# Kernel optimization log

Hardware: AMD Instinct MI355X
Metric: run time of the kernel (lower is better)

Reference implementation:

```python
import math
import jax, jax.numpy as jnp
import numpy as np

D_MODEL = 1024
H_HEADS = 16
D_K = D_MODEL // H_HEADS


def setup_inputs() -> dict:
    key = jax.random.key(0)
    ks = jax.random.split(key, 7)
    B, L = 4, 2048
    q = jax.random.normal(ks[0], (B, L, D_MODEL), dtype=jnp.float32)
    k = jax.random.normal(ks[1], (B, L, D_MODEL), dtype=jnp.float32)
    v = jax.random.normal(ks[2], (B, L, D_MODEL), dtype=jnp.float32)
    mask = jnp.ones((1, L, L), dtype=jnp.int32)
    # nn.Linear(d_model, d_model, bias=False) weights, shape (out, in)
    s = 1.0 / math.sqrt(D_MODEL)
    W_q = jax.random.uniform(ks[3], (D_MODEL, D_MODEL), jnp.float32, -s, s)
    W_k = jax.random.uniform(ks[4], (D_MODEL, D_MODEL), jnp.float32, -s, s)
    W_v = jax.random.uniform(ks[5], (D_MODEL, D_MODEL), jnp.float32, -s, s)
    W_o = jax.random.uniform(ks[6], (D_MODEL, D_MODEL), jnp.float32, -s, s)
    return {"q": q, "k": k, "v": v, "mask": mask,
            "W_q": W_q, "W_k": W_k, "W_v": W_v, "W_o": W_o}


def reference(q, k, v, mask, W_q, W_k, W_v, W_o):
    B, Lq, _ = q.shape
    # projections (Linear: x @ W.T) then split heads -> (B, H, L, d_k)
    def split_heads(x):
        return x.reshape(B, -1, H_HEADS, D_K).transpose(0, 2, 1, 3)
    Q = split_heads(jnp.einsum('bsd,ed->bse', q, W_q))
    K = split_heads(jnp.einsum('bsd,ed->bse', k, W_k))
    V = split_heads(jnp.einsum('bsd,ed->bse', v, W_v))
    # scores: (B, H, Lq, Lk)
    scores = jnp.einsum('bhqd,bhkd->bhqk', Q, K) / math.sqrt(D_K)
    m = mask[:, None, :, :]  # (1, 1, Lq, Lk) broadcast
    scores = jnp.where(m == 0, -jnp.inf, scores)
    weights = jax.nn.softmax(scores, axis=-1)
    attn = jnp.einsum('bhqk,bhkd->bhqd', weights, V)  # (B, H, Lq, d_v)
    attn = attn.transpose(0, 2, 1, 3).reshape(B, Lq, D_MODEL)
    return jnp.einsum('bse,de->bsd', attn, W_o)
```

## Files before the change

### kernel.cpp

```cpp
#include <hip/hip_runtime.h>
#include <hip/hip_bf16.h>


typedef unsigned short u16;
typedef float f32x4  __attribute__((ext_vector_type(4)));
typedef float f32x16 __attribute__((ext_vector_type(16)));
typedef short s16x8  __attribute__((ext_vector_type(8)));
typedef unsigned u32x4 __attribute__((ext_vector_type(4)));
typedef __bf16 bf16x8 __attribute__((ext_vector_type(8)));

#define QSCL 0.18033688011112042f

__device__ __forceinline__ u16 f2b(float f) {
    union { float f; unsigned u; } x; x.f = f;
    unsigned r = x.u + 0x7fffu + ((x.u >> 16) & 1u);
    return (u16)(r >> 16);
}

__device__ __forceinline__ f32x4 MF(s16x8 a, s16x8 b, f32x4 c) {
    return __builtin_amdgcn_mfma_f32_16x16x32_bf16(
        __builtin_bit_cast(bf16x8, a), __builtin_bit_cast(bf16x8, b), c, 0, 0, 0);
}
__device__ __forceinline__ f32x16 MF32(s16x8 a, s16x8 b, f32x16 c) {
    return __builtin_amdgcn_mfma_f32_32x32x16_bf16(
        __builtin_bit_cast(bf16x8, a), __builtin_bit_cast(bf16x8, b), c, 0, 0, 0);
}
__device__ __forceinline__ unsigned cvtpk(float lo, float hi) {
    unsigned r;
    asm("v_cvt_pk_bf16_f32 %0, %1, %2" : "=v"(r) : "v"(lo), "v"(hi));
    return r;
}
__device__ __forceinline__ void swap32(unsigned &a, unsigned &b) {
    asm volatile("v_permlane32_swap_b32 %0, %1" : "+v"(a), "+v"(b));
}
__device__ __forceinline__ float expa(float x) {
    float r;
    asm("v_exp_f32 %0, %1" : "=v"(r) : "v"(x));
    return r;
}
__device__ __forceinline__ void g2l16(const u16* g, u16* lbase) {
    __builtin_amdgcn_global_load_lds((const __attribute__((address_space(1))) void*)g,
                                     (__attribute__((address_space(3))) void*)lbase, 16, 0, 0);
}

__global__ __launch_bounds__(256)
void mask_flags(const int* __restrict__ mask, int* __restrict__ mflag) {
    __shared__ int anyz;
    if (threadIdx.x == 0) anyz = 0;
    __syncthreads();
    const int qt = blockIdx.x >> 4, kt = blockIdx.x & 15;
    int local = 0;
#pragma unroll
    for (int q = 0; q < 16; ++q) {
        int e4 = q * 256 + threadIdx.x;
        int r = e4 >> 5, cc = (e4 & 31) * 4;
        int4 mv = *(const int4*)(mask + (size_t)(qt * 128 + r) * 2048 + kt * 128 + cc);
        local |= (mv.x == 0) | (mv.y == 0) | (mv.z == 0) | (mv.w == 0);
    }
    if (local) atomicOr(&anyz, 1);
    __syncthreads();
    if (threadIdx.x == 0) mflag[blockIdx.x] = anyz;
}

__global__ __launch_bounds__(256)
void convert_all(const float* __restrict__ q, const float* __restrict__ k,
                 const float* __restrict__ v, const float* __restrict__ Wq,
                 const float* __restrict__ Wk, const float* __restrict__ Wv,
                 const float* __restrict__ Wo, u16* __restrict__ Abf,
                 u16* __restrict__ Wbf) {
    const size_t NQKV = 25165824;
    const size_t NCH  = 3670016;
    for (size_t cidx = (size_t)blockIdx.x * 256 + threadIdx.x; cidx < NCH;
         cidx += (size_t)gridDim.x * 256) {
        size_t e = cidx * 8;
        const float* src; u16* dst; float scl = 1.f;
        if (e < NQKV) {
            src = (e < 8388608) ? q + e
                : (e < 16777216) ? k + (e - 8388608) : v + (e - 16777216);
            dst = Abf + e;
        } else {
            size_t o = e - NQKV;
            if (o < 1048576)      { src = Wq + o; scl = QSCL; }
            else if (o < 2097152) { src = Wk + (o - 1048576); }
            else if (o < 3145728) { src = Wv + (o - 2097152); }
            else                  { src = Wo + (o - 3145728); }
            dst = Wbf + o;
        }
        float4 a = *(const float4*)(src);
        float4 b = *(const float4*)(src + 4);
        ushort4 p0, p1;
        p0.x = f2b(a.x * scl); p0.y = f2b(a.y * scl);
        p0.z = f2b(a.z * scl); p0.w = f2b(a.w * scl);
        p1.x = f2b(b.x * scl); p1.y = f2b(b.y * scl);
        p1.z = f2b(b.z * scl); p1.w = f2b(b.w * scl);
        *(ushort4*)dst = p0; *(ushort4*)(dst + 4) = p1;
    }
}

__global__ __launch_bounds__(256)
void gemm_qkv_fast(const u16* __restrict__ Abf, const u16* __restrict__ Wbf,
                   u16* __restrict__ Qh, u16* __restrict__ Kf, u16* __restrict__ Vf) {
    __shared__ __align__(16) u16 As[128 * 32];
    __shared__ __align__(16) u16 Bs[128 * 32];
    const int z = blockIdx.z;
    const u16* A = Abf + (size_t)z * (8192 * 1024);
    const u16* W = Wbf + (size_t)z * (1024 * 1024);
    const int tid = threadIdx.x, l = tid & 63, w = tid >> 6;
    const int g = l >> 4, c = l & 15;
    const int m0 = blockIdx.y * 128, n0 = blockIdx.x * 128;
    const int wr = (w >> 1) * 64, wc = (w & 1) * 64;

    f32x4 acc[4][4];
#pragma unroll
    for (int i = 0; i < 4; ++i)
#pragma unroll
        for (int j = 0; j < 4; ++j)
#pragma unroll
            for (int e = 0; e < 4; ++e) acc[i][j][e] = 0.f;

    const u16* Ag = A + (size_t)(m0 + w * 32 + (l >> 2)) * 1024 + (l & 3) * 8;
    const u16* Wg = W + (size_t)(n0 + w * 32 + (l >> 2)) * 1024 + (l & 3) * 8;
    u16* Al = As + w * 1024;
    u16* Bl = Bs + w * 1024;

    for (int kt = 0; kt < 32; ++kt) {
        __syncthreads();
        g2l16(Ag + kt * 32,         Al);
        g2l16(Ag + kt * 32 + 16384, Al + 512);
        g2l16(Wg + kt * 32,         Bl);
        g2l16(Wg + kt * 32 + 16384, Bl + 512);
        __syncthreads();
        s16x8 af[4], bf[4];
#pragma unroll
        for (int i = 0; i < 4; ++i) {
            af[i] = *(const s16x8*)(As + (wr + i * 16 + c) * 32 + g * 8);
            bf[i] = *(const s16x8*)(Bs + (wc + i * 16 + c) * 32 + g * 8);
        }
#pragma unroll
        for (int mi = 0; mi < 4; ++mi)
#pragma unroll
            for (int ni = 0; ni < 4; ++ni)
                acc[mi][ni] = MF(af[mi], bf[ni], acc[mi][ni]);
    }

    if (z == 0) {
#pragma unroll
        for (int mi = 0; mi < 4; ++mi)
#pragma unroll
            for (int ni = 0; ni < 4; ++ni)
#pragma unroll
                for (int j = 0; j < 4; ++j) {
                    int row = m0 + wr + mi * 16 + g * 4 + j;
                    int col = n0 + wc + ni * 16 + c;
                    int b = row >> 11, sl = row & 2047;
                    int h = col >> 6, d = col & 63;
                    Qh[(((size_t)(b * 16 + h)) * 2048 + sl) * 64 + d] = f2b(acc[mi][ni][j]);
                }
    } else if (z == 1) {
#pragma unroll
        for (int mi = 0; mi < 4; ++mi)
#pragma unroll
            for (int ni = 0; ni < 4; ++ni)
#pragma unroll
                for (int j = 0; j < 4; ++j) {
                    int row = m0 + wr + mi * 16 + g * 4 + j;
                    int col = n0 + wc + ni * 16 + c;
                    int b = row >> 11, kk = row & 2047;
                    int h = col >> 6, d = col & 63;
                    size_t off = (size_t)(b * 16 + h) * 131072
                               + (size_t)(((kk >> 5) * 4 + (d >> 4))) * 512
                               + ((kk & 31) + 32 * ((d >> 3) & 1)) * 8 + (d & 7);
                    Kf[off] = f2b(acc[mi][ni][j]);
                }
    } else {
#pragma unroll
        for (int mi = 0; mi < 4; ++mi)
#pragma unroll
            for (int ni = 0; ni < 4; ++ni) {
                int key0 = m0 + wr + mi * 16 + g * 4;
                int col  = n0 + wc + ni * 16 + c;
                int b = key0 >> 11, kk0 = key0 & 2047;
                int h = col >> 6, d = col & 63;
                size_t off = (size_t)(b * 16 + h) * 131072
                           + (size_t)((kk0 >> 6) * 8 + (d >> 5) * 4 + ((kk0 >> 4) & 3)) * 512
                           + (((kk0 >> 3) & 1) * 32 + (d & 31)) * 8 + (kk0 & 7);
                ushort4 pk;
                pk.x = f2b(acc[mi][ni][0]); pk.y = f2b(acc[mi][ni][1]);
                pk.z = f2b(acc[mi][ni][2]); pk.w = f2b(acc[mi][ni][3]);
                *(ushort4*)(Vf + off) = pk;
            }
    }
}

__global__ __launch_bounds__(256)
void gemm_out_fast(const u16* __restrict__ Ab, const u16* __restrict__ W,
                   float* __restrict__ Cout) {
    __shared__ __align__(16) u16 As[128 * 32];
    __shared__ __align__(16) u16 Bs[128 * 32];
    const int tid = threadIdx.x, l = tid & 63, w = tid >> 6;
    const int g = l >> 4, c = l & 15;
    const int m0 = blockIdx.y * 128, n0 = blockIdx.x * 128;
    const int wr = (w >> 1) * 64, wc = (w & 1) * 64;

    f32x4 acc[4][4];
#pragma unroll
    for (int i = 0; i < 4; ++i)
#pragma unroll
        for (int j = 0; j < 4; ++j)
#pragma unroll
            for (int e = 0; e < 4; ++e) acc[i][j][e] = 0.f;

    const u16* Ag = Ab + (size_t)(m0 + w * 32 + (l >> 2)) * 1024 + (l & 3) * 8;
    const u16* Wg = W  + (size_t)(n0 + w * 32 + (l >> 2)) * 1024 + (l & 3) * 8;
    u16* Al = As + w * 1024;
    u16* Bl = Bs + w * 1024;

    for (int kt = 0; kt < 32; ++kt) {
        __syncthreads();
        g2l16(Ag + kt * 32,         Al);
        g2l16(Ag + kt * 32 + 16384, Al + 512);
        g2l16(Wg + kt * 32,         Bl);
        g2l16(Wg + kt * 32 + 16384, Bl + 512);
        __syncthreads();
        s16x8 af[4], bf[4];
#pragma unroll
        for (int i = 0; i < 4; ++i) {
            af[i] = *(const s16x8*)(As + (wr + i * 16 + c) * 32 + g * 8);
            bf[i] = *(const s16x8*)(Bs + (wc + i * 16 + c) * 32 + g * 8);
        }
#pragma unroll
        for (int mi = 0; mi < 4; ++mi)
#pragma unroll
            for (int ni = 0; ni < 4; ++ni)
                acc[mi][ni] = MF(af[mi], bf[ni], acc[mi][ni]);
    }

#pragma unroll
    for (int mi = 0; mi < 4; ++mi)
#pragma unroll
        for (int ni = 0; ni < 4; ++ni)
#pragma unroll
            for (int j = 0; j < 4; ++j) {
                int row = m0 + wr + mi * 16 + g * 4 + j;
                int col = n0 + wc + ni * 16 + c;
                Cout[(size_t)row * 1024 + col] = acc[mi][ni][j];
            }
}

__global__ __launch_bounds__(256)
void flash_attn(const u16* __restrict__ Qh, const u16* __restrict__ Kf,
                const u16* __restrict__ Vf, const int* __restrict__ mask,
                const int* __restrict__ mflag, u16* __restrict__ attnB) {
    __shared__ __align__(16) u16 KV[2][2][8][512];

    const int tid = threadIdx.x, w = tid >> 6, l = tid & 63;
    const int hi = l >> 5, q32 = l & 31;
    const int bh = blockIdx.x, qt = blockIdx.y;
    const size_t base = (size_t)bh * (2048 * 64);
    const u16* Qp = Qh + base;
    const u16* Kp = Kf + base;
    const u16* Vp = Vf + base;
    const int qrow_w = qt * 128 + w * 32;

    s16x8 Qf[4];
#pragma unroll
    for (int s = 0; s < 4; ++s)
        Qf[s] = *(const s16x8*)(Qp + (size_t)(qrow_w + q32) * 64 + s * 16 + hi * 8);

    f32x16 z16;
#pragma unroll
    for (int r = 0; r < 16; ++r) z16[r] = 0.f;
    f32x16 oA = z16, oB = z16;
    float la[4] = {0.f, 0.f, 0.f, 0.f};

    auto stage = [&](int buf, int kt) {
        const u16* ks = Kp + (size_t)(kt * 8 + w * 2) * 512 + l * 8;
        const u16* vs = Vp + (size_t)(kt * 8 + w * 2) * 512 + l * 8;
        g2l16(ks,       &KV[buf][0][w * 2][0]);
        g2l16(ks + 512, &KV[buf][0][w * 2 + 1][0]);
        g2l16(vs,       &KV[buf][1][w * 2][0]);
        g2l16(vs + 512, &KV[buf][1][w * 2 + 1][0]);
    };
    stage(0, 0);

    for (int kt = 0; kt < 32; ++kt) {
        const int cur = kt & 1;
        __syncthreads();
        if (kt < 31) stage(cur ^ 1, kt + 1);

        __builtin_amdgcn_s_setprio(1);
        f32x16 sA, sB;
        {
            s16x8 ka = *(const s16x8*)&KV[cur][0][0][l * 8];
            s16x8 kb = *(const s16x8*)&KV[cur][0][4][l * 8];
            sA = MF32(ka, Qf[0], z16);
            sB = MF32(kb, Qf[0], z16);
        }
#pragma unroll
        for (int s = 1; s < 4; ++s) {
            s16x8 ka = *(const s16x8*)&KV[cur][0][s][l * 8];
            s16x8 kb = *(const s16x8*)&KV[cur][0][4 + s][l * 8];
            sA = MF32(ka, Qf[s], sA);
            sB = MF32(kb, Qf[s], sB);
        }
        __builtin_amdgcn_s_setprio(0);

        if (mflag[qt * 16 + (kt >> 1)] != 0) {
            const int qr = qrow_w + q32, kr0 = kt * 64;
#pragma unroll
            for (int r = 0; r < 16; ++r) {
                int key = (r & 3) + 8 * (r >> 2) + 4 * hi;
                if (mask[(size_t)qr * 2048 + kr0 + key] == 0)      sA[r] = -1e30f;
                if (mask[(size_t)qr * 2048 + kr0 + 32 + key] == 0) sB[r] = -1e30f;
            }
        }

#pragma unroll
        for (int r = 0; r < 16; ++r) { sA[r] = expa(sA[r]); la[r & 3] += sA[r]; }
#pragma unroll
        for (int r = 0; r < 16; ++r) { sB[r] = expa(sB[r]); la[r & 3] += sB[r]; }

        s16x8 Xp[4];
        {
            u32x4 t;
            unsigned a0 = cvtpk(sA[0], sA[1]),   a1 = cvtpk(sA[2], sA[3]);
            unsigned b0 = cvtpk(sA[4], sA[5]),   b1 = cvtpk(sA[6], sA[7]);
            swap32(a0, b0); swap32(a1, b1);
            t.x = a0; t.y = a1; t.z = b0; t.w = b1; Xp[0] = __builtin_bit_cast(s16x8, t);
            unsigned c0 = cvtpk(sA[8], sA[9]),   c1 = cvtpk(sA[10], sA[11]);
            unsigned d0 = cvtpk(sA[12], sA[13]), d1 = cvtpk(sA[14], sA[15]);
            swap32(c0, d0); swap32(c1, d1);
            t.x = c0; t.y = c1; t.z = d0; t.w = d1; Xp[1] = __builtin_bit_cast(s16x8, t);
            unsigned e0 = cvtpk(sB[0], sB[1]),   e1 = cvtpk(sB[2], sB[3]);
            unsigned f0 = cvtpk(sB[4], sB[5]),   f1 = cvtpk(sB[6], sB[7]);
            swap32(e0, f0); swap32(e1, f1);
            t.x = e0; t.y = e1; t.z = f0; t.w = f1; Xp[2] = __builtin_bit_cast(s16x8, t);
            unsigned g0 = cvtpk(sB[8], sB[9]),   g1 = cvtpk(sB[10], sB[11]);
            unsigned h0 = cvtpk(sB[12], sB[13]), h1 = cvtpk(sB[14], sB[15]);
            swap32(g0, h0); swap32(g1, h1);
            t.x = g0; t.y = g1; t.z = h0; t.w = h1; Xp[3] = __builtin_bit_cast(s16x8, t);
        }

        __builtin_amdgcn_s_setprio(1);
#pragma unroll
        for (int ks = 0; ks < 4; ++ks) {
            s16x8 v0 = *(const s16x8*)&KV[cur][1][ks][l * 8];
            s16x8 v1 = *(const s16x8*)&KV[cur][1][4 + ks][l * 8];
            oA = MF32(Xp[ks], v0, oA);
            oB = MF32(Xp[ks], v1, oB);
        }
        __builtin_amdgcn_s_setprio(0);
    }

    float ls = (la[0] + la[1]) + (la[2] + la[3]);
    ls += __shfl_xor(ls, 32);

    const int b = bh >> 4, h = bh & 15;
#pragma unroll
    for (int r = 0; r < 16; ++r) {
        int qloc = (r & 3) + 8 * (r >> 2) + 4 * hi;
        float lr = __shfl(ls, qloc);
        float inv = __builtin_amdgcn_rcpf(lr);
        int row = qt * 128 + w * 32 + qloc;
        u16* dst = attnB + ((size_t)b * 2048 + row) * 1024 + h * 64 + q32;
        dst[0]  = f2b(oA[r] * inv);
        dst[32] = f2b(oB[r] * inv);
    }
}

extern "C" void kernel_launch(void* const* d_in, const int* in_sizes, int n_in,
                              void* d_out, int out_size, void* d_ws, size_t ws_size,
                              hipStream_t stream) {
    const float* q    = (const float*)d_in[0];
    const float* k    = (const float*)d_in[1];
    const float* v    = (const float*)d_in[2];
    const int*   mask = (const int*)d_in[3];
    const float* Wq   = (const float*)d_in[4];
    const float* Wk   = (const float*)d_in[5];
    const float* Wv   = (const float*)d_in[6];
    const float* Wo   = (const float*)d_in[7];

    char* ws = (char*)d_ws;
    u16* Abf   = (u16*)(ws);
    u16* Wbf   = (u16*)(ws + (48u << 20));
    u16* Qh    = (u16*)(ws + (56u << 20));
    u16* Kf    = (u16*)(ws + (72u << 20));
    u16* Vf    = (u16*)(ws + (88u << 20));
    u16* attnB = (u16*)(ws);
    int* mflag = (int*)(ws + (104u << 20));

    mask_flags<<<dim3(256), dim3(256), 0, stream>>>(mask, mflag);
    convert_all<<<dim3(2048), dim3(256), 0, stream>>>(q, k, v, Wq, Wk, Wv, Wo, Abf, Wbf);
    gemm_qkv_fast<<<dim3(8, 64, 3), dim3(256), 0, stream>>>(Abf, Wbf, Qh, Kf, Vf);
    flash_attn<<<dim3(64, 16), dim3(256), 0, stream>>>(Qh, Kf, Vf, mask, mflag, attnB);
    gemm_out_fast<<<dim3(8, 64), dim3(256), 0, stream>>>(attnB, Wbf + 3145728, (float*)d_out);
}
```

Baseline: 235.4 us.

## Give each attention wave two query sub-tiles and swap GEMM grid axes

The flash attention kernel now runs 128 threads with each wave owning 64 query rows (two 32-row sub-tiles). Each K/V fragment read from shared memory is therefore reused for twice as many MFMAs, and each wave stages four K/V slabs instead of two. It also hoists a per-block any-mask check out of the loop. The two projection GEMMs swap their grid x/y mapping so that consecutive blocks walk along M rather than N, which changes L2 reuse of the weight tiles. The trade-off is higher register pressure and fewer waves per block in attention.

```diff
diff --git a/kernel.cpp b/kernel.cpp
--- a/kernel.cpp
+++ b/kernel.cpp
@@ -107,7 +107,7 @@
     const u16* W = Wbf + (size_t)z * (1024 * 1024);
     const int tid = threadIdx.x, l = tid & 63, w = tid >> 6;
     const int g = l >> 4, c = l & 15;
-    const int m0 = blockIdx.y * 128, n0 = blockIdx.x * 128;
+    const int m0 = blockIdx.x * 128, n0 = blockIdx.y * 128;
     const int wr = (w >> 1) * 64, wc = (w & 1) * 64;
 
     f32x4 acc[4][4];
@@ -199,7 +199,7 @@
     __shared__ __align__(16) u16 Bs[128 * 32];
     const int tid = threadIdx.x, l = tid & 63, w = tid >> 6;
     const int g = l >> 4, c = l & 15;
-    const int m0 = blockIdx.y * 128, n0 = blockIdx.x * 128;
+    const int m0 = blockIdx.x * 128, n0 = blockIdx.y * 128;
     const int wr = (w >> 1) * 64, wc = (w & 1) * 64;
 
     f32x4 acc[4][4];
@@ -247,7 +247,7 @@
             }
 }
 
-__global__ __launch_bounds__(256)
+__global__ __launch_bounds__(128)
 void flash_attn(const u16* __restrict__ Qh, const u16* __restrict__ Kf,
                 const u16* __restrict__ Vf, const int* __restrict__ mask,
                 const int* __restrict__ mflag, u16* __restrict__ attnB) {
@@ -260,26 +260,33 @@
     const u16* Qp = Qh + base;
     const u16* Kp = Kf + base;
     const u16* Vp = Vf + base;
-    const int qrow_w = qt * 128 + w * 32;
-
-    s16x8 Qf[4];
-#pragma unroll
-    for (int s = 0; s < 4; ++s)
-        Qf[s] = *(const s16x8*)(Qp + (size_t)(qrow_w + q32) * 64 + s * 16 + hi * 8);
+    const int qrow_w = qt * 128 + w * 64;
+
+    int anyflag = 0;
+#pragma unroll
+    for (int i = 0; i < 16; ++i) anyflag |= mflag[qt * 16 + i];
+
+    s16x8 Qf0[4], Qf1[4];
+#pragma unroll
+    for (int s = 0; s < 4; ++s) {
+        Qf0[s] = *(const s16x8*)(Qp + (size_t)(qrow_w + q32) * 64 + s * 16 + hi * 8);
+        Qf1[s] = *(const s16x8*)(Qp + (size_t)(qrow_w + 32 + q32) * 64 + s * 16 + hi * 8);
+    }
 
     f32x16 z16;
 #pragma unroll
     for (int r = 0; r < 16; ++r) z16[r] = 0.f;
-    f32x16 oA = z16, oB = z16;
-    float la[4] = {0.f, 0.f, 0.f, 0.f};
+    f32x16 oA0 = z16, oB0 = z16, oA1 = z16, oB1 = z16;
+    float la0[4] = {0.f, 0.f, 0.f, 0.f}, la1[4] = {0.f, 0.f, 0.f, 0.f};
 
     auto stage = [&](int buf, int kt) {
-        const u16* ks = Kp + (size_t)(kt * 8 + w * 2) * 512 + l * 8;
-        const u16* vs = Vp + (size_t)(kt * 8 + w * 2) * 512 + l * 8;
-        g2l16(ks,       &KV[buf][0][w * 2][0]);
-        g2l16(ks + 512, &KV[buf][0][w * 2 + 1][0]);
-        g2l16(vs,       &KV[buf][1][w * 2][0]);
-        g2l16(vs + 512, &KV[buf][1][w * 2 + 1][0]);
+        const u16* ks = Kp + (size_t)(kt * 8 + w * 4) * 512 + l * 8;
+        const u16* vs = Vp + (size_t)(kt * 8 + w * 4) * 512 + l * 8;
+#pragma unroll
+        for (int i = 0; i < 4; ++i) {
+            g2l16(ks + i * 512, &KV[buf][0][w * 4 + i][0]);
+            g2l16(vs + i * 512, &KV[buf][1][w * 4 + i][0]);
+        }
     };
     stage(0, 0);
 
@@ -289,56 +296,81 @@
         if (kt < 31) stage(cur ^ 1, kt + 1);
 
         __builtin_amdgcn_s_setprio(1);
-        f32x16 sA, sB;
+        f32x16 sA0, sB0, sA1, sB1;
         {
             s16x8 ka = *(const s16x8*)&KV[cur][0][0][l * 8];
             s16x8 kb = *(const s16x8*)&KV[cur][0][4][l * 8];
-            sA = MF32(ka, Qf[0], z16);
-            sB = MF32(kb, Qf[0], z16);
+            sA0 = MF32(ka, Qf0[0], z16); sA1 = MF32(ka, Qf1[0], z16);
+            sB0 = MF32(kb, Qf0[0], z16); sB1 = MF32(kb, Qf1[0], z16);
         }
 #pragma unroll
         for (int s = 1; s < 4; ++s) {
             s16x8 ka = *(const s16x8*)&KV[cur][0][s][l * 8];
             s16x8 kb = *(const s16x8*)&KV[cur][0][4 + s][l * 8];
-            sA = MF32(ka, Qf[s], sA);
-            sB = MF32(kb, Qf[s], sB);
+            sA0 = MF32(ka, Qf0[s], sA0); sA1 = MF32(ka, Qf1[s], sA1);
+            sB0 = MF32(kb, Qf0[s], sB0); sB1 = MF32(kb, Qf1[s], sB1);
         }
         __builtin_amdgcn_s_setprio(0);
 
-        if (mflag[qt * 16 + (kt >> 1)] != 0) {
-            const int qr = qrow_w + q32, kr0 = kt * 64;
+        if (anyflag && mflag[qt * 16 + (kt >> 1)] != 0) {
+            const int kr0 = kt * 64;
+            const int qr0 = qrow_w + q32, qr1 = qrow_w + 32 + q32;
 #pragma unroll
             for (int r = 0; r < 16; ++r) {
                 int key = (r & 3) + 8 * (r >> 2) + 4 * hi;
-                if (mask[(size_t)qr * 2048 + kr0 + key] == 0)      sA[r] = -1e30f;
-                if (mask[(size_t)qr * 2048 + kr0 + 32 + key] == 0) sB[r] = -1e30f;
+                if (mask[(size_t)qr0 * 2048 + kr0 + key] == 0)      sA0[r] = -1e30f;
+                if (mask[(size_t)qr0 * 2048 + kr0 + 32 + key] == 0) sB0[r] = -1e30f;
+                if (mask[(size_t)qr1 * 2048 + kr0 + key] == 0)      sA1[r] = -1e30f;
+                if (mask[(size_t)qr1 * 2048 + kr0 + 32 + key] == 0) sB1[r] = -1e30f;
             }
         }
 
-#pragma unroll
-        for (int r = 0; r < 16; ++r) { sA[r] = expa(sA[r]); la[r & 3] += sA[r]; }
-#pragma unroll
-        for (int r = 0; r < 16; ++r) { sB[r] = expa(sB[r]); la[r & 3] += sB[r]; }
-
-        s16x8 Xp[4];
+        s16x8 Xp0[4], Xp1[4];
+#pragma unroll
+        for (int r = 0; r < 16; ++r) { sA0[r] = expa(sA0[r]); la0[r & 3] += sA0[r]; }
+#pragma unroll
+        for (int r = 0; r < 16; ++r) { sB0[r] = expa(sB0[r]); la0[r & 3] += sB0[r]; }
         {
             u32x4 t;
-            unsigned a0 = cvtpk(sA[0], sA[1]),   a1 = cvtpk(sA[2], sA[3]);
-            unsigned b0 = cvtpk(sA[4], sA[5]),   b1 = cvtpk(sA[6], sA[7]);
+            unsigned a0 = cvtpk(sA0[0], sA0[1]),   a1 = cvtpk(sA0[2], sA0[3]);
+            unsigned b0 = cvtpk(sA0[4], sA0[5]),   b1 = cvtpk(sA0[6], sA0[7]);
             swap32(a0, b0); swap32(a1, b1);
-            t.x = a0; t.y = a1; t.z = b0; t.w = b1; Xp[0] = __builtin_bit_cast(s16x8, t);
-            unsigned c0 = cvtpk(sA[8], sA[9]),   c1 = cvtpk(sA[10], sA[11]);
-            unsigned d0 = cvtpk(sA[12], sA[13]), d1 = cvtpk(sA[14], sA[15]);
+            t.x = a0; t.y = a1; t.z = b0; t.w = b1; Xp0[0] = __builtin_bit_cast(s16x8, t);
+            unsigned c0 = cvtpk(sA0[8], sA0[9]),   c1 = cvtpk(sA0[10], sA0[11]);
+            unsigned d0 = cvtpk(sA0[12], sA0[13]), d1 = cvtpk(sA0[14], sA0[15]);
             swap32(c0, d0); swap32(c1, d1);
-            t.x = c0; t.y = c1; t.z = d0; t.w = d1; Xp[1] = __builtin_bit_cast(s16x8, t);
-            unsigned e0 = cvtpk(sB[0], sB[1]),   e1 = cvtpk(sB[2], sB[3]);
-            unsigned f0 = cvtpk(sB[4], sB[5]),   f1 = cvtpk(sB[6], sB[7]);
+            t.x = c0; t.y = c1; t.z = d0; t.w = d1; Xp0[1] = __builtin_bit_cast(s16x8, t);
+            unsigned e0 = cvtpk(sB0[0], sB0[1]),   e1 = cvtpk(sB0[2], sB0[3]);
+            unsigned f0 = cvtpk(sB0[4], sB0[5]),   f1 = cvtpk(sB0[6], sB0[7]);
             swap32(e0, f0); swap32(e1, f1);
-            t.x = e0; t.y = e1; t.z = f0; t.w = f1; Xp[2] = __builtin_bit_cast(s16x8, t);
-            unsigned g0 = cvtpk(sB[8], sB[9]),   g1 = cvtpk(sB[10], sB[11]);
-            unsigned h0 = cvtpk(sB[12], sB[13]), h1 = cvtpk(sB[14], sB[15]);
+            t.x = e0; t.y = e1; t.z = f0; t.w = f1; Xp0[2] = __builtin_bit_cast(s16x8, t);
+            unsigned g0 = cvtpk(sB0[8], sB0[9]),   g1 = cvtpk(sB0[10], sB0[11]);
+            unsigned h0 = cvtpk(sB0[12], sB0[13]), h1 = cvtpk(sB0[14], sB0[15]);
             swap32(g0, h0); swap32(g1, h1);
-            t.x = g0; t.y = g1; t.z = h0; t.w = h1; Xp[3] = __builtin_bit_cast(s16x8, t);
+            t.x = g0; t.y = g1; t.z = h0; t.w = h1; Xp0[3] = __builtin_bit_cast(s16x8, t);
+        }
+#pragma unroll
+        for (int r = 0; r < 16; ++r) { sA1[r] = expa(sA1[r]); la1[r & 3] += sA1[r]; }
+#pragma unroll
+        for (int r = 0; r < 16; ++r) { sB1[r] = expa(sB1[r]); la1[r & 3] += sB1[r]; }
+        {
+            u32x4 t;
+            unsigned a0 = cvtpk(sA1[0], sA1[1]),   a1 = cvtpk(sA1[2], sA1[3]);
+            unsigned b0 = cvtpk(sA1[4], sA1[5]),   b1 = cvtpk(sA1[6], sA1[7]);
+            swap32(a0, b0); swap32(a1, b1);
+            t.x = a0; t.y = a1; t.z = b0; t.w = b1; Xp1[0] = __builtin_bit_cast(s16x8, t);
+            unsigned c0 = cvtpk(sA1[8], sA1[9]),   c1 = cvtpk(sA1[10], sA1[11]);
+            unsigned d0 = cvtpk(sA1[12], sA1[13]), d1 = cvtpk(sA1[14], sA1[15]);
+            swap32(c0, d0); swap32(c1, d1);
+            t.x = c0; t.y = c1; t.z = d0; t.w = d1; Xp1[1] = __builtin_bit_cast(s16x8, t);
+            unsigned e0 = cvtpk(sB1[0], sB1[1]),   e1 = cvtpk(sB1[2], sB1[3]);
+            unsigned f0 = cvtpk(sB1[4], sB1[5]),   f1 = cvtpk(sB1[6], sB1[7]);
+            swap32(e0, f0); swap32(e1, f1);
+            t.x = e0; t.y = e1; t.z = f0; t.w = f1; Xp1[2] = __builtin_bit_cast(s16x8, t);
+            unsigned g0 = cvtpk(sB1[8], sB1[9]),   g1 = cvtpk(sB1[10], sB1[11]);
+            unsigned h0 = cvtpk(sB1[12], sB1[13]), h1 = cvtpk(sB1[14], sB1[15]);
+            swap32(g0, h0); swap32(g1, h1);
+            t.x = g0; t.y = g1; t.z = h0; t.w = h1; Xp1[3] = __builtin_bit_cast(s16x8, t);
         }
 
         __builtin_amdgcn_s_setprio(1);
@@ -346,25 +378,38 @@
         for (int ks = 0; ks < 4; ++ks) {
             s16x8 v0 = *(const s16x8*)&KV[cur][1][ks][l * 8];
             s16x8 v1 = *(const s16x8*)&KV[cur][1][4 + ks][l * 8];
-            oA = MF32(Xp[ks], v0, oA);
-            oB = MF32(Xp[ks], v1, oB);
+            oA0 = MF32(Xp0[ks], v0, oA0); oA1 = MF32(Xp1[ks], v0, oA1);
+            oB0 = MF32(Xp0[ks], v1, oB0); oB1 = MF32(Xp1[ks], v1, oB1);
         }
         __builtin_amdgcn_s_setprio(0);
     }
 
-    float ls = (la[0] + la[1]) + (la[2] + la[3]);
-    ls += __shfl_xor(ls, 32);
-
     const int b = bh >> 4, h = bh & 15;
-#pragma unroll
-    for (int r = 0; r < 16; ++r) {
-        int qloc = (r & 3) + 8 * (r >> 2) + 4 * hi;
-        float lr = __shfl(ls, qloc);
-        float inv = __builtin_amdgcn_rcpf(lr);
-        int row = qt * 128 + w * 32 + qloc;
-        u16* dst = attnB + ((size_t)b * 2048 + row) * 1024 + h * 64 + q32;
-        dst[0]  = f2b(oA[r] * inv);
-        dst[32] = f2b(oB[r] * inv);
+    {
+        float ls = (la0[0] + la0[1]) + (la0[2] + la0[3]);
+        ls += __shfl_xor(ls, 32);
+#pragma unroll
+        for (int r = 0; r < 16; ++r) {
+            int qloc = (r & 3) + 8 * (r >> 2) + 4 * hi;
+            float inv = __builtin_amdgcn_rcpf(__shfl(ls, qloc));
+            int row = qrow_w + qloc;
+            u16* dst = attnB + ((size_t)b * 2048 + row) * 1024 + h * 64 + q32;
+            dst[0]  = f2b(oA0[r] * inv);
+            dst[32] = f2b(oB0[r] * inv);
+        }
+    }
+    {
+        float ls = (la1[0] + la1[1]) + (la1[2] + la1[3]);
+        ls += __shfl_xor(ls, 32);
+#pragma unroll
+        for (int r = 0; r < 16; ++r) {
+            int qloc = (r & 3) + 8 * (r >> 2) + 4 * hi;
+            float inv = __builtin_amdgcn_rcpf(__shfl(ls, qloc));
+            int row = qrow_w + 32 + qloc;
+            u16* dst = attnB + ((size_t)b * 2048 + row) * 1024 + h * 64 + q32;
+            dst[0]  = f2b(oA1[r] * inv);
+            dst[32] = f2b(oB1[r] * inv);
+        }
     }
 }
 
@@ -391,7 +436,7 @@
 
     mask_flags<<<dim3(256), dim3(256), 0, stream>>>(mask, mflag);
     convert_all<<<dim3(2048), dim3(256), 0, stream>>>(q, k, v, Wq, Wk, Wv, Wo, Abf, Wbf);
-    gemm_qkv_fast<<<dim3(8, 64, 3), dim3(256), 0, stream>>>(Abf, Wbf, Qh, Kf, Vf);
-    flash_attn<<<dim3(64, 16), dim3(256), 0, stream>>>(Qh, Kf, Vf, mask, mflag, attnB);
-    gemm_out_fast<<<dim3(8, 64), dim3(256), 0, stream>>>(attnB, Wbf + 3145728, (float*)d_out);
-}
+    gemm_qkv_fast<<<dim3(64, 8, 3), dim3(256), 0, stream>>>(Abf, Wbf, Qh, Kf, Vf);
+    flash_attn<<<dim3(64, 16), dim3(128), 0, stream>>>(Qh, Kf, Vf, mask, mflag, attnB);
+    gemm_out_fast<<<dim3(64, 8), dim3(256), 0, stream>>>(attnB, Wbf + 3145728, (float*)d_out);
+}
```

After: 241.3 us. 1.02x slower.
